# Kernel optimization log

Measured on AMD Instinct MI355X. Metric: run time of the kernel, lower is better.

Reference implementation:

```python
import jax, jax.numpy as jnp
from jax import lax
import numpy as np

B, N, C, NPOINT, K = 8, 4096, 64, 1024, 32
EPS = 1e-5
SLOPE = 0.1  # leakyrelu negative_slope


def setup_inputs() -> dict:
    key = jax.random.key(0)
    ks = jax.random.split(key, 8)
    d = {
        "xyz": jax.random.normal(ks[0], (B, N, 3), jnp.float32),
        "features": jax.random.normal(ks[1], (B, N, C), jnp.float32),
    }
    for i, n in enumerate(["w_t", "w1_0", "w2_0", "w1_1", "w2_1"]):
        d[n] = jax.random.normal(ks[2 + i], (C, C), jnp.float32) * 0.05
    for n in ["b_t", "b1_0", "b2_0", "b1_1", "b2_1"]:
        d[n] = jnp.zeros((C,), jnp.float32)
    for n in ["g_t", "g1_0", "g2_0", "g1_1", "g2_1"]:
        d[n] = jnp.ones((C,), jnp.float32)
    for n in ["beta_t", "beta1_0", "beta2_0", "beta1_1", "beta2_1"]:
        d[n] = jnp.zeros((C,), jnp.float32)
    return d


def leaky(x):
    return jnp.where(x >= 0, x, SLOPE * x)


def conv1(x, w, b):  # x: [M, Cin, K], w: [Cout, Cin] (1x1 conv)
    return jnp.einsum('mck,oc->mok', x, w) + b[None, :, None]


def bn(x, g, be):  # training-mode BatchNorm1d over (batch, spatial)
    mean = x.mean(axis=(0, 2), keepdims=True)
    var = x.var(axis=(0, 2), keepdims=True)
    return g[None, :, None] * (x - mean) / jnp.sqrt(var + EPS) + be[None, :, None]


def fps(xyz, npoint):
    """Farthest point sampling, deterministic start at index 0. -> [B, npoint] int32"""
    b, n, _ = xyz.shape
    def step(carry, _):
        dist, far = carry
        centroid = jnp.take_along_axis(xyz, far[:, None, None], axis=1)  # [B,1,3]
        d = jnp.sum((xyz - centroid) ** 2, -1)  # [B,N]
        dist = jnp.minimum(dist, d)
        return (dist, jnp.argmax(dist, -1)), far
    init = (jnp.full((b, n), 1e10, xyz.dtype), jnp.zeros((b,), jnp.int32))
    _, idxs = lax.scan(step, init, None, length=npoint)  # [npoint, B]
    return idxs.T


def sqdist(src, dst):  # [B,S,3],[B,N,3] -> [B,S,N]
    d = -2.0 * jnp.einsum('bsc,bnc->bsn', src, dst)
    d += jnp.sum(src ** 2, -1)[:, :, None]
    d += jnp.sum(dst ** 2, -1)[:, None, :]
    return d


def resblock(x, w1, b1, g1, be1, w2, b2, g2, be2):
    h = leaky(bn(conv1(x, w1, b1), g1, be1))
    h = bn(conv1(h, w2, b2), g2, be2)
    return leaky(h + x)


def reference(xyz, features, w_t, b_t, g_t, beta_t,
              w1_0, b1_0, g1_0, beta1_0, w2_0, b2_0, g2_0, beta2_0,
              w1_1, b1_1, g1_1, beta1_1, w2_1, b2_1, g2_1, beta2_1):
    fps_idx = fps(xyz, NPOINT)                                   # [B,S]
    new_xyz = jnp.take_along_axis(xyz, fps_idx[:, :, None], axis=1)  # [B,S,3]
    d = sqdist(new_xyz, xyz)                                     # [B,S,N]
    _, idx = lax.top_k(-d, K)                                    # k smallest -> [B,S,K]
    grouped = jax.vmap(lambda f, i: f[i])(features, idx)         # [B,S,K,C]
    x = grouped.transpose(0, 1, 3, 2).reshape(B * NPOINT, C, K)  # [B*S, C, K]
    x = leaky(bn(conv1(x, w_t, b_t), g_t, beta_t))
    x = resblock(x, w1_0, b1_0, g1_0, beta1_0, w2_0, b2_0, g2_0, beta2_0)
    x = resblock(x, w1_1, b1_1, g1_1, beta1_1, w2_1, b2_1, g2_1, beta2_1)
    nf = x.reshape(B, NPOINT, C, K).transpose(0, 2, 1, 3)        # [B,C,S,K]
    sub_features = nf.max(axis=-1)                               # [B,C,S]
    return (new_xyz.transpose(0, 2, 1), sub_features)
```

## Files before the change

### kernel.cpp

```cpp
#include <hip/hip_runtime.h>
#include <stdint.h>

#define NB 8
#define NN 4096
#define NC 64
#define NS 1024
#define NK 32
#define NQ (NB*NS)
#define NP (NQ*NK)
#define EPSBN 1e-5f

typedef unsigned long long u64;
typedef unsigned short u16;
typedef float v2f __attribute__((ext_vector_type(2)));
typedef short bf8_t __attribute__((ext_vector_type(8)));
typedef float f4_t __attribute__((ext_vector_type(4)));

__device__ __forceinline__ float lrelu(float x){ return x >= 0.0f ? x : 0.1f*x; }

__device__ __forceinline__ unsigned int fkey(float d){
    unsigned int fb = __float_as_uint(d);
    return (fb & 0x80000000u) ? ~fb : (fb | 0x80000000u);
}
__device__ __forceinline__ unsigned f2bf(float f){
    unsigned u = __float_as_uint(f);
    return (u + 0x7fffu + ((u >> 16) & 1u)) >> 16;
}
__device__ __forceinline__ float bflo(unsigned u){ return __uint_as_float(u << 16); }
__device__ __forceinline__ float bfhi(unsigned u){ return __uint_as_float(u & 0xffff0000u); }

__device__ __forceinline__ int wave_incl_add(int x){
    int v = x;
    {int o=__builtin_amdgcn_update_dpp(0,v,0x111,0xf,0xf,true); v+=o;}
    {int o=__builtin_amdgcn_update_dpp(0,v,0x112,0xf,0xf,true); v+=o;}
    {int o=__builtin_amdgcn_update_dpp(0,v,0x114,0xf,0xf,true); v+=o;}
    {int o=__builtin_amdgcn_update_dpp(0,v,0x118,0xf,0xf,true); v+=o;}
    {int o=__builtin_amdgcn_update_dpp(0,v,0x142,0xa,0xf,true); v+=o;}
    {int o=__builtin_amdgcn_update_dpp(0,v,0x143,0xc,0xf,true); v+=o;}
    return v;
}
__device__ __forceinline__ float row_sum16(float x){
    int v = __float_as_int(x);
    {int o=__builtin_amdgcn_update_dpp(0,v,0x111,0xf,0xf,true); v=__float_as_int(__int_as_float(v)+__int_as_float(o));}
    {int o=__builtin_amdgcn_update_dpp(0,v,0x112,0xf,0xf,true); v=__float_as_int(__int_as_float(v)+__int_as_float(o));}
    {int o=__builtin_amdgcn_update_dpp(0,v,0x114,0xf,0xf,true); v=__float_as_int(__int_as_float(v)+__int_as_float(o));}
    {int o=__builtin_amdgcn_update_dpp(0,v,0x118,0xf,0xf,true); v=__float_as_int(__int_as_float(v)+__int_as_float(o));}
    return __int_as_float(v);
}
__device__ __forceinline__ double wave_max_d(double x){
    int lo = __double2loint(x), hi = __double2hiint(x);
    #define FPS_STG(ctl) { \
        int nl=__builtin_amdgcn_update_dpp(lo,lo,ctl,0xf,0xf,false); \
        int nh=__builtin_amdgcn_update_dpp(hi,hi,ctl,0xf,0xf,false); \
        double mx=fmax(__hiloint2double(hi,lo), __hiloint2double(nh,nl)); \
        lo=__double2loint(mx); hi=__double2hiint(mx); }
    FPS_STG(0x111) FPS_STG(0x112) FPS_STG(0x114) FPS_STG(0x118) FPS_STG(0x142) FPS_STG(0x143)
    #undef FPS_STG
    int flo = __builtin_amdgcn_readlane(lo, 63);
    int fhi = __builtin_amdgcn_readlane(hi, 63);
    return __hiloint2double(fhi, flo);
}

__global__ __launch_bounds__(256,1) void fps_kernel(const float* __restrict__ xyz,
                                                    float* __restrict__ out0,
                                                    float* __restrict__ nxyz,
                                                    const float* __restrict__ features,
                                                    u16* __restrict__ fbf)
{
    if (blockIdx.x >= NB){
        const int cb = blockIdx.x - NB;
        const float4* src = (const float4*)features;
        uint2* dst = (uint2*)fbf;
        for (int i = cb*256 + threadIdx.x; i < NB*NN*NC/4; i += 512*256){
            float4 v = src[i];
            uint2 pk;
            pk.x = f2bf(v.x) | (f2bf(v.y) << 16);
            pk.y = f2bf(v.z) | (f2bf(v.w) << 16);
            dst[i] = pk;
        }
        return;
    }
    __shared__ float sX[NN], sY[NN], sZ[NN];
    __shared__ double slots[2][4];
    __shared__ int sFar[NS];
    const int b = blockIdx.x, t = threadIdx.x;
    const int lane = t & 63, wv = t >> 6;
    const float* base = xyz + (size_t)b*NN*3;
    for (int i = t; i < NN; i += 256){
        const float* pp = base + 3*i;
        sX[i] = pp[0]; sY[i] = pp[1]; sZ[i] = pp[2];
    }
    __syncthreads();
    v2f PX[8], PY[8], PZ[8], D[8];
    int LO[16];
    const int pb = t*16;
    #pragma unroll
    for (int j = 0; j < 8; ++j){
        PX[j] = (v2f){ sX[pb+2*j], sX[pb+2*j+1] };
        PY[j] = (v2f){ sY[pb+2*j], sY[pb+2*j+1] };
        PZ[j] = (v2f){ sZ[pb+2*j], sZ[pb+2*j+1] };
        D[j]  = (v2f){ 1e10f, 1e10f };
    }
    #pragma unroll
    for (int j = 0; j < 16; ++j) LO[j] = (int)(~(unsigned)(pb + j));
    int far = 0;
    float cx = sX[0], cy = sY[0], cz = sZ[0];
    for (int s = 0; s < NS; ++s){
        if (t == 255) sFar[s] = far;
        double best;
        {
            #pragma clang fp contract(off)
            v2f cx2 = (v2f){cx, cx}, cy2 = (v2f){cy, cy}, cz2 = (v2f){cz, cz};
            best = -1.0;
            #pragma unroll
            for (int j = 0; j < 8; ++j){
                v2f dx = PX[j] - cx2;
                v2f dy = PY[j] - cy2;
                v2f dz = PZ[j] - cz2;
                v2f dd = (dx*dx + dy*dy) + dz*dz;
                v2f nd = __builtin_elementwise_min(D[j], dd);
                D[j] = nd;
                best = fmax(best, __hiloint2double(__float_as_int(nd.x), LO[2*j]));
                best = fmax(best, __hiloint2double(__float_as_int(nd.y), LO[2*j+1]));
            }
        }
        double wb = wave_max_d(best);
        const int par = s & 1;
        if (lane == 0) slots[par][wv] = wb;
        __syncthreads();
        double s0 = slots[par][0], s1 = slots[par][1];
        double s2 = slots[par][2], s3 = slots[par][3];
        double mm = fmax(fmax(s0, s1), fmax(s2, s3));
        far = (int)(~(unsigned)__double2loint(mm));
        cx = sX[far]; cy = sY[far]; cz = sZ[far];
    }
    __syncthreads();
    for (int s = t; s < NS; s += 256){
        const int f = sFar[s];
        const float x = sX[f], y = sY[f], z = sZ[f];
        float* npq = nxyz + ((size_t)b*NS + s)*3;
        npq[0]=x; npq[1]=y; npq[2]=z;
        out0[(b*3+0)*NS+s]=x; out0[(b*3+1)*NS+s]=y; out0[(b*3+2)*NS+s]=z;
    }
}

__global__ __launch_bounds__(256,2) void knn_kernel(const float* __restrict__ xyz,
                                                    const float* __restrict__ nxyz,
                                                    int* __restrict__ kidx)
{
    const int t = threadIdx.x, lane = t & 63, w = t >> 6;
    const int q = blockIdx.x*4 + w;
    const int b = q >> 10;
    const float* base = xyz + (size_t)b*NN*3;
    const float* qp = nxyz + (size_t)q*3;
    const float qx = qp[0], qy = qp[1], qz = qp[2];
    const float qsq = __fadd_rn(__fadd_rn(__fmul_rn(qx,qx),__fmul_rn(qy,qy)),__fmul_rn(qz,qz));

    unsigned int key[64];
    #pragma unroll
    for (int i = 0; i < 64; ++i){
        const int idx = (i<<6) + lane;
        const float* pp = base + 3*idx;
        float x = pp[0], y = pp[1], z = pp[2];
        float dot = __fadd_rn(__fadd_rn(__fmul_rn(qx,x),__fmul_rn(qy,y)),__fmul_rn(qz,z));
        float psq = __fadd_rn(__fadd_rn(__fmul_rn(x,x),__fmul_rn(y,y)),__fmul_rn(z,z));
        float d = __fadd_rn(__fadd_rn(__fmul_rn(-2.0f,dot),qsq),psq);
        key[i] = fkey(d);
    }
    unsigned int pref = 0; int need = 32;
    for (int bit = 31; bit >= 0; --bit){
        const unsigned int bound = 1u << bit;
        int c = 0;
        #pragma unroll
        for (int i = 0; i < 64; ++i) c += ((key[i] ^ pref) < bound) ? 1 : 0;
        int tot = __builtin_amdgcn_readlane(wave_incl_add(c), 63);
        if (tot < need){ need -= tot; pref |= bound; }
    }
    const unsigned int T = pref;
    int cl = 0;
    #pragma unroll
    for (int i = 0; i < 64; ++i) cl += (key[i] < T) ? 1 : 0;
    int incl_cl = wave_incl_add(cl);
    int clx = incl_cl - cl;
    int tiebase = __builtin_amdgcn_readlane(incl_cl, 63);
    int* oq = kidx + (size_t)q*NK;
    int pos = clx;
    #pragma unroll
    for (int i = 0; i < 64; ++i){
        if (key[i] < T){ oq[pos] = (i<<6) + lane; ++pos; }
    }
    int tcount = 0;
    for (int i = 0; i < 64 && tcount < need; ++i){
        u64 m = __ballot(key[i] == T);
        int myrank = (int)__popcll(m & ((1ull << lane) - 1ull));
        if ((key[i] == T) && (tcount + myrank < need))
            oq[tiebase + tcount + myrank] = (i<<6) + lane;
        tcount += (int)__popcll(m);
    }
}

__global__ __launch_bounds__(256) void wtrans_kernel(const float* __restrict__ w0,
    const float* __restrict__ w1, const float* __restrict__ w2,
    const float* __restrict__ w3, const float* __restrict__ w4,
    u16* __restrict__ dst)
{
    const float* s;
    switch (blockIdx.x){
        case 0: s = w0; break; case 1: s = w1; break; case 2: s = w2; break;
        case 3: s = w3; break; default: s = w4; break;
    }
    u16* d = dst + (size_t)blockIdx.x*4096;
    for (int i = threadIdx.x; i < 4096; i += 256){
        const int f = i >> 9, lane = (i >> 3) & 63, j = i & 7;
        const int mt = f >> 1, h = f & 1;
        const int o = mt*16 + (lane & 15);
        const int c = h*32 + (lane >> 4)*8 + j;
        d[i] = (u16)f2bf(s[o*64 + c]);
    }
}

__global__ __launch_bounds__(1024) void finalize_kernel(const float* __restrict__ pin,
    const float* __restrict__ g, const float* __restrict__ beta, float* __restrict__ aff)
{
    __shared__ float l1[1024];
    const int t = threadIdx.x;
    const int stat = t & 127, seg = t >> 7;
    float S = 0.0f;
    #pragma unroll 8
    for (int r = seg*128; r < seg*128 + 128; ++r) S += pin[r*128 + stat];
    l1[t] = S;
    __syncthreads();
    if (t < 128){
        float s = l1[t] + l1[128+t] + l1[256+t] + l1[384+t]
                + l1[512+t] + l1[640+t] + l1[768+t] + l1[896+t];
        l1[t] = s;
    }
    __syncthreads();
    if (t < 64){
        float mean = l1[t] * (1.0f/(float)NP);
        float var  = fmaxf(l1[64+t] * (1.0f/(float)NP) - mean*mean, 0.0f);
        float sc = g[t] * rsqrtf(var + EPSBN);
        aff[t]    = sc;
        aff[64+t] = beta[t] - mean*sc;
    }
}

template<int ACT>
__global__ __launch_bounds__(256,3) void conv_mfma_kernel(const u16* __restrict__ in,
    u16* __restrict__ out, const u16* __restrict__ wfrag, const float* __restrict__ bias,
    const float* __restrict__ aff, float* __restrict__ pout)
{
    __shared__ float sStat[4*128];
    const int t = threadIdx.x, lane = t & 63, wv = t >> 6;
    const int n = lane & 15, q = lane >> 4;
    const int bb = blockIdx.x;

    float scr[16], shr[16];
    if (ACT){
        #pragma unroll
        for (int h = 0; h < 2; ++h){
            float4 a0 = *(const float4*)(aff + h*32 + q*8);
            float4 a1 = *(const float4*)(aff + h*32 + q*8 + 4);
            float4 b0 = *(const float4*)(aff + 64 + h*32 + q*8);
            float4 b1 = *(const float4*)(aff + 64 + h*32 + q*8 + 4);
            scr[h*8+0]=a0.x; scr[h*8+1]=a0.y; scr[h*8+2]=a0.z; scr[h*8+3]=a0.w;
            scr[h*8+4]=a1.x; scr[h*8+5]=a1.y; scr[h*8+6]=a1.z; scr[h*8+7]=a1.w;
            shr[h*8+0]=b0.x; shr[h*8+1]=b0.y; shr[h*8+2]=b0.z; shr[h*8+3]=b0.w;
            shr[h*8+4]=b1.x; shr[h*8+5]=b1.y; shr[h*8+6]=b1.z; shr[h*8+7]=b1.w;
        }
    }
    bf8_t wf[8];
    #pragma unroll
    for (int f = 0; f < 8; ++f)
        wf[f] = *(const bf8_t*)(wfrag + (f*64 + lane)*8);
    f4_t bv[4];
    #pragma unroll
    for (int mt = 0; mt < 4; ++mt)
        bv[mt] = *(const f4_t*)(bias + mt*16 + q*4);

    float st1[16], st2[16];
    #pragma unroll
    for (int e = 0; e < 16; ++e){ st1[e] = 0.0f; st2[e] = 0.0f; }

    #pragma unroll
    for (int i = 0; i < 4; ++i){
        const int p0 = bb*256 + wv*64 + i*16;
        const u16* row = in + (size_t)(p0 + n)*64;
        bf8_t bf0, bf1;
        if (ACT){
            union { unsigned u[4]; bf8_t v; } B0, B1;
            uint4 r0 = *(const uint4*)(row + q*8);
            uint4 r1 = *(const uint4*)(row + 32 + q*8);
            const unsigned ra[4] = {r0.x, r0.y, r0.z, r0.w};
            const unsigned rb[4] = {r1.x, r1.y, r1.z, r1.w};
            #pragma unroll
            for (int d = 0; d < 4; ++d){
                float x0 = bflo(ra[d]), x1 = bfhi(ra[d]);
                float y0 = fmaf(scr[2*d],   x0, shr[2*d]);   y0 = lrelu(y0);
                float y1 = fmaf(scr[2*d+1], x1, shr[2*d+1]); y1 = lrelu(y1);
                B0.u[d] = f2bf(y0) | (f2bf(y1) << 16);
                float z0 = bflo(rb[d]), z1 = bfhi(rb[d]);
                float w0 = fmaf(scr[8+2*d],   z0, shr[8+2*d]);   w0 = lrelu(w0);
                float w1 = fmaf(scr[8+2*d+1], z1, shr[8+2*d+1]); w1 = lrelu(w1);
                B1.u[d] = f2bf(w0) | (f2bf(w1) << 16);
            }
            bf0 = B0.v; bf1 = B1.v;
        } else {
            bf0 = *(const bf8_t*)(row + q*8);
            bf1 = *(const bf8_t*)(row + 32 + q*8);
        }
        f4_t acc[4];
        #pragma unroll
        for (int mt = 0; mt < 4; ++mt){
            acc[mt] = (f4_t){0.f,0.f,0.f,0.f};
            acc[mt] = __builtin_amdgcn_mfma_f32_16x16x32_bf16(wf[mt*2+0], bf0, acc[mt], 0,0,0);
            acc[mt] = __builtin_amdgcn_mfma_f32_16x16x32_bf16(wf[mt*2+1], bf1, acc[mt], 0,0,0);
        }
        u16* orow = out + (size_t)(p0 + n)*64;
        #pragma unroll
        for (int mt = 0; mt < 4; ++mt){
            float v0 = acc[mt].x + bv[mt].x;
            float v1 = acc[mt].y + bv[mt].y;
            float v2 = acc[mt].z + bv[mt].z;
            float v3 = acc[mt].w + bv[mt].w;
            st1[mt*4+0] += v0; st2[mt*4+0] += v0*v0;
            st1[mt*4+1] += v1; st2[mt*4+1] += v1*v1;
            st1[mt*4+2] += v2; st2[mt*4+2] += v2*v2;
            st1[mt*4+3] += v3; st2[mt*4+3] += v3*v3;
            uint2 pk;
            pk.x = f2bf(v0) | (f2bf(v1) << 16);
            pk.y = f2bf(v2) | (f2bf(v3) << 16);
            *(uint2*)(orow + mt*16 + q*4) = pk;
        }
    }
    #pragma unroll
    for (int e = 0; e < 16; ++e){
        float r1 = row_sum16(st1[e]);
        float r2 = row_sum16(st2[e]);
        if (n == 15){
            const int ch = (e >> 2)*16 + q*4 + (e & 3);
            sStat[wv*128 + ch]      = r1;
            sStat[wv*128 + 64 + ch] = r2;
        }
    }
    __syncthreads();
    if (t < 128){
        float s = sStat[t] + sStat[128+t] + sStat[256+t] + sStat[384+t];
        pout[(size_t)bb*128 + t] = s;
    }
}

__global__ __launch_bounds__(256,3) void gconv_mfma_kernel(const u16* __restrict__ fbf,
    const int* __restrict__ kidx, u16* __restrict__ out,
    const u16* __restrict__ wfrag, const float* __restrict__ bias,
    float* __restrict__ pout)
{
    __shared__ float sStat[4*128];
    const int t = threadIdx.x, lane = t & 63, wv = t >> 6;
    const int n = lane & 15, q = lane >> 4;
    const int bb = blockIdx.x;

    bf8_t wf[8];
    #pragma unroll
    for (int f = 0; f < 8; ++f)
        wf[f] = *(const bf8_t*)(wfrag + (f*64 + lane)*8);
    f4_t bv[4];
    #pragma unroll
    for (int mt = 0; mt < 4; ++mt)
        bv[mt] = *(const f4_t*)(bias + mt*16 + q*4);

    float st1[16], st2[16];
    #pragma unroll
    for (int e = 0; e < 16; ++e){ st1[e] = 0.0f; st2[e] = 0.0f; }

    #pragma unroll
    for (int i = 0; i < 4; ++i){
        const int p0 = bb*256 + wv*64 + i*16;
        const int p = p0 + n;
        const int b = p >> 15;
        const int idx = kidx[p];
        const u16* frow = fbf + ((size_t)b*NN + idx)*NC;
        bf8_t bf0 = *(const bf8_t*)(frow + q*8);
        bf8_t bf1 = *(const bf8_t*)(frow + 32 + q*8);
        f4_t acc[4];
        #pragma unroll
        for (int mt = 0; mt < 4; ++mt){
            acc[mt] = (f4_t){0.f,0.f,0.f,0.f};
            acc[mt] = __builtin_amdgcn_mfma_f32_16x16x32_bf16(wf[mt*2+0], bf0, acc[mt], 0,0,0);
            acc[mt] = __builtin_amdgcn_mfma_f32_16x16x32_bf16(wf[mt*2+1], bf1, acc[mt], 0,0,0);
        }
        u16* orow = out + (size_t)p*64;
        #pragma unroll
        for (int mt = 0; mt < 4; ++mt){
            float v0 = acc[mt].x + bv[mt].x;
            float v1 = acc[mt].y + bv[mt].y;
            float v2 = acc[mt].z + bv[mt].z;
            float v3 = acc[mt].w + bv[mt].w;
            st1[mt*4+0] += v0; st2[mt*4+0] += v0*v0;
            st1[mt*4+1] += v1; st2[mt*4+1] += v1*v1;
            st1[mt*4+2] += v2; st2[mt*4+2] += v2*v2;
            st1[mt*4+3] += v3; st2[mt*4+3] += v3*v3;
            uint2 pk;
            pk.x = f2bf(v0) | (f2bf(v1) << 16);
            pk.y = f2bf(v2) | (f2bf(v3) << 16);
            *(uint2*)(orow + mt*16 + q*4) = pk;
        }
    }
    #pragma unroll
    for (int e = 0; e < 16; ++e){
        float r1 = row_sum16(st1[e]);
        float r2 = row_sum16(st2[e]);
        if (n == 15){
            const int ch = (e >> 2)*16 + q*4 + (e & 3);
            sStat[wv*128 + ch]      = r1;
            sStat[wv*128 + 64 + ch] = r2;
        }
    }
    __syncthreads();
    if (t < 128){
        float s = sStat[t] + sStat[128+t] + sStat[256+t] + sStat[384+t];
        pout[(size_t)bb*128 + t] = s;
    }
}

__global__ __launch_bounds__(256,2) void resid_kernel(const u16* __restrict__ v,
    const u16* __restrict__ yt, u16* __restrict__ x2,
    const float* __restrict__ affV, const float* __restrict__ affY)
{
    const int t = threadIdx.x;
    const int dc = t & 31, rg = t >> 5;
    const int c0 = dc*2, c1 = c0 + 1;
    const float va0 = affV[c0], vb0 = affV[64+c0];
    const float va1 = affV[c1], vb1 = affV[64+c1];
    const float ya0 = affY[c0], yb0 = affY[64+c0];
    const float ya1 = affY[c1], yb1 = affY[64+c1];
    const unsigned* vp = (const unsigned*)v;
    const unsigned* yp = (const unsigned*)yt;
    unsigned* xp = (unsigned*)x2;
    const size_t base = (size_t)blockIdx.x*512;
    #pragma unroll 4
    for (int r = rg; r < 512; r += 8){
        const size_t e = (base + r)*32 + dc;
        unsigned uv = vp[e], uy = yp[e];
        float r0 = lrelu(fmaf(va0, bflo(uv), vb0) + lrelu(fmaf(ya0, bflo(uy), yb0)));
        float r1 = lrelu(fmaf(va1, bfhi(uv), vb1) + lrelu(fmaf(ya1, bfhi(uy), yb1)));
        xp[e] = f2bf(r0) | (f2bf(r1) << 16);
    }
}

__global__ __launch_bounds__(256,2) void final_kernel(const u16* __restrict__ v2,
    const u16* __restrict__ x2, const float* __restrict__ aff,
    float* __restrict__ out1)
{
    const int t = threadIdx.x;
    const int dc = t & 31, sg = t >> 5;
    const int c0 = dc*2, c1 = c0 + 1;
    const float a0 = aff[c0], s0 = aff[64+c0];
    const float a1 = aff[c1], s1 = aff[64+c1];
    const int s = blockIdx.x*8 + sg;
    const unsigned* vp = (const unsigned*)v2;
    const unsigned* xp = (const unsigned*)x2;
    float m0 = -3.0e38f, m1 = -3.0e38f;
    #pragma unroll 8
    for (int kk = 0; kk < 32; ++kk){
        const size_t e = ((size_t)s*32 + kk)*32 + dc;
        unsigned uv = vp[e], ux = xp[e];
        m0 = fmaxf(m0, lrelu(fmaf(a0, bflo(uv), s0) + bflo(ux)));
        m1 = fmaxf(m1, lrelu(fmaf(a1, bfhi(uv), s1) + bfhi(ux)));
    }
    const int b = s >> 10, sl = s & 1023;
    out1[((size_t)b*NC + c0)*NS + sl] = m0;
    out1[((size_t)b*NC + c1)*NS + sl] = m1;
}

extern "C" void kernel_launch(void* const* d_in, const int* in_sizes, int n_in,
                              void* d_out, int out_size, void* d_ws, size_t ws_size,
                              hipStream_t stream)
{
    const float* xyz      = (const float*)d_in[0];
    const float* features = (const float*)d_in[1];
    const float* w_t    = (const float*)d_in[2];
    const float* w1_0   = (const float*)d_in[3];
    const float* w2_0   = (const float*)d_in[4];
    const float* w1_1   = (const float*)d_in[5];
    const float* w2_1   = (const float*)d_in[6];
    const float* b_t    = (const float*)d_in[7];
    const float* b1_0   = (const float*)d_in[8];
    const float* b2_0   = (const float*)d_in[9];
    const float* b1_1   = (const float*)d_in[10];
    const float* b2_1   = (const float*)d_in[11];
    const float* g_t    = (const float*)d_in[12];
    const float* g1_0   = (const float*)d_in[13];
    const float* g2_0   = (const float*)d_in[14];
    const float* g1_1   = (const float*)d_in[15];
    const float* g2_1   = (const float*)d_in[16];
    const float* beta_t  = (const float*)d_in[17];
    const float* beta1_0 = (const float*)d_in[18];
    const float* beta2_0 = (const float*)d_in[19];
    const float* beta1_1 = (const float*)d_in[20];
    const float* beta2_1 = (const float*)d_in[21];

    float* out = (float*)d_out;

    float* nxyz = (float*)d_ws;
    int*   kidx = (int*)(nxyz + 24576);
    float* pT   = (float*)(kidx + NP);
    float* p10  = pT  + 131072;
    float* p20  = p10 + 131072;
    float* p11  = p20 + 131072;
    float* p21  = p11 + 131072;
    float* affT  = p21 + 131072;
    float* aff10 = affT + 128;
    float* aff20 = aff10 + 128;
    float* aff11 = aff20 + 128;
    float* aff21 = aff11 + 128;
    u16*  bwt  = (u16*)(aff21 + 128);
    u16*  buf0 = bwt + 5*4096;
    u16*  buf1 = buf0 + (size_t)NP*NC;
    u16*  buf2 = buf1 + (size_t)NP*NC;
    u16*  fbf  = buf2;

    wtrans_kernel<<<5, 256, 0, stream>>>(w_t, w1_0, w2_0, w1_1, w2_1, bwt);
    fps_kernel<<<NB + 512, 256, 0, stream>>>(xyz, out, nxyz, features, fbf);
    knn_kernel<<<NQ/4, 256, 0, stream>>>(xyz, nxyz, kidx);

    gconv_mfma_kernel<<<1024, 256, 0, stream>>>(fbf, kidx, buf1,
                                                bwt + 0*4096, b_t, pT);
    finalize_kernel<<<1, 1024, 0, stream>>>(pT, g_t, beta_t, affT);
    conv_mfma_kernel<1><<<1024, 256, 0, stream>>>(buf1, buf0, bwt + 1*4096, b1_0,
                                                  affT, p10);
    finalize_kernel<<<1, 1024, 0, stream>>>(p10, g1_0, beta1_0, aff10);
    conv_mfma_kernel<1><<<1024, 256, 0, stream>>>(buf0, buf2, bwt + 2*4096, b2_0,
                                                  aff10, p20);
    finalize_kernel<<<1, 1024, 0, stream>>>(p20, g2_0, beta2_0, aff20);
    resid_kernel<<<512, 256, 0, stream>>>(buf2, buf1, buf0, aff20, affT);
    conv_mfma_kernel<0><<<1024, 256, 0, stream>>>(buf0, buf1, bwt + 3*4096, b1_1,
                                                  nullptr, p11);
    finalize_kernel<<<1, 1024, 0, stream>>>(p11, g1_1, beta1_1, aff11);
    conv_mfma_kernel<1><<<1024, 256, 0, stream>>>(buf1, buf2, bwt + 4*4096, b2_1,
                                                  aff11, p21);
    finalize_kernel<<<1, 1024, 0, stream>>>(p21, g2_1, beta2_1, aff21);
    final_kernel<<<1024, 256, 0, stream>>>(buf2, buf0, aff21,
                                           out + (size_t)NB*3*NS);
}
```

Baseline: 905.8 us.

## Fuse BN finalize into conv tails, fold residual into conv, merge weight prep

```diff
diff --git a/kernel.cpp b/kernel.cpp
--- a/kernel.cpp
+++ b/kernel.cpp
@@ -61,12 +61,71 @@
     return __hiloint2double(fhi, flo);
 }
 
+__device__ __forceinline__ void tail_finalize(const float* __restrict__ pin,
+    const float* __restrict__ g, const float* __restrict__ beta,
+    float* __restrict__ affout, int* __restrict__ ticket, int t)
+{
+    __shared__ int isTail;
+    __shared__ float l1[1024];
+    __threadfence();
+    __syncthreads();
+    if (t == 0) isTail = ((atomicAdd(ticket, 1) & 1023) == 1023) ? 1 : 0;
+    __syncthreads();
+    if (!isTail) return;
+    __threadfence();
+    const float4* p4 = (const float4*)pin;
+    const int col4 = t & 31, seg = t >> 5;
+    float4 S = {0.f, 0.f, 0.f, 0.f};
+    #pragma unroll 8
+    for (int r = seg*128; r < seg*128 + 128; ++r){
+        float4 v = p4[(size_t)r*32 + col4];
+        S.x += v.x; S.y += v.y; S.z += v.z; S.w += v.w;
+    }
+    l1[seg*128 + col4*4 + 0] = S.x;
+    l1[seg*128 + col4*4 + 1] = S.y;
+    l1[seg*128 + col4*4 + 2] = S.z;
+    l1[seg*128 + col4*4 + 3] = S.w;
+    __syncthreads();
+    if (t < 128){
+        float s = l1[t] + l1[128+t] + l1[256+t] + l1[384+t]
+                + l1[512+t] + l1[640+t] + l1[768+t] + l1[896+t];
+        l1[t] = s;
+    }
+    __syncthreads();
+    if (t < 64){
+        float mean = l1[t] * (1.0f/(float)NP);
+        float var  = fmaxf(l1[64+t] * (1.0f/(float)NP) - mean*mean, 0.0f);
+        float sc = g[t] * rsqrtf(var + EPSBN);
+        affout[t]    = sc;
+        affout[64+t] = beta[t] - mean*sc;
+    }
+}
+
 __global__ __launch_bounds__(256,1) void fps_kernel(const float* __restrict__ xyz,
-                                                    float* __restrict__ out0,
-                                                    float* __restrict__ nxyz,
-                                                    const float* __restrict__ features,
-                                                    u16* __restrict__ fbf)
-{
+    float* __restrict__ out0, float* __restrict__ nxyz,
+    const float* __restrict__ features, u16* __restrict__ fbf,
+    const float* __restrict__ w0, const float* __restrict__ w1,
+    const float* __restrict__ w2, const float* __restrict__ w3,
+    const float* __restrict__ w4, u16* __restrict__ bwt, int* __restrict__ tickets)
+{
+    if (blockIdx.x >= NB + 512){
+        const int wb = blockIdx.x - (NB + 512);
+        if (wb == 0 && threadIdx.x < 8) tickets[threadIdx.x] = 0;
+        const float* s;
+        switch (wb){
+            case 0: s = w0; break; case 1: s = w1; break; case 2: s = w2; break;
+            case 3: s = w3; break; default: s = w4; break;
+        }
+        u16* d = bwt + (size_t)wb*4096;
+        for (int i = threadIdx.x; i < 4096; i += 256){
+            const int f = i >> 9, lane = (i >> 3) & 63, j = i & 7;
+            const int mt = f >> 1, h = f & 1;
+            const int o = mt*16 + (lane & 15);
+            const int c = h*32 + (lane >> 4)*8 + j;
+            d[i] = (u16)f2bf(s[o*64 + c]);
+        }
+        return;
+    }
     if (blockIdx.x >= NB){
         const int cb = blockIdx.x - NB;
         const float4* src = (const float4*)features;
@@ -199,56 +258,15 @@
     }
 }
 
-__global__ __launch_bounds__(256) void wtrans_kernel(const float* __restrict__ w0,
-    const float* __restrict__ w1, const float* __restrict__ w2,
-    const float* __restrict__ w3, const float* __restrict__ w4,
-    u16* __restrict__ dst)
-{
-    const float* s;
-    switch (blockIdx.x){
-        case 0: s = w0; break; case 1: s = w1; break; case 2: s = w2; break;
-        case 3: s = w3; break; default: s = w4; break;
-    }
-    u16* d = dst + (size_t)blockIdx.x*4096;
-    for (int i = threadIdx.x; i < 4096; i += 256){
-        const int f = i >> 9, lane = (i >> 3) & 63, j = i & 7;
-        const int mt = f >> 1, h = f & 1;
-        const int o = mt*16 + (lane & 15);
-        const int c = h*32 + (lane >> 4)*8 + j;
-        d[i] = (u16)f2bf(s[o*64 + c]);
-    }
-}
-
-__global__ __launch_bounds__(1024) void finalize_kernel(const float* __restrict__ pin,
-    const float* __restrict__ g, const float* __restrict__ beta, float* __restrict__ aff)
-{
-    __shared__ float l1[1024];
-    const int t = threadIdx.x;
-    const int stat = t & 127, seg = t >> 7;
-    float S = 0.0f;
-    #pragma unroll 8
-    for (int r = seg*128; r < seg*128 + 128; ++r) S += pin[r*128 + stat];
-    l1[t] = S;
-    __syncthreads();
-    if (t < 128){
-        float s = l1[t] + l1[128+t] + l1[256+t] + l1[384+t]
-                + l1[512+t] + l1[640+t] + l1[768+t] + l1[896+t];
-        l1[t] = s;
-    }
-    __syncthreads();
-    if (t < 64){
-        float mean = l1[t] * (1.0f/(float)NP);
-        float var  = fmaxf(l1[64+t] * (1.0f/(float)NP) - mean*mean, 0.0f);
-        float sc = g[t] * rsqrtf(var + EPSBN);
-        aff[t]    = sc;
-        aff[64+t] = beta[t] - mean*sc;
-    }
-}
-
 template<int ACT>
-__global__ __launch_bounds__(256,3) void conv_mfma_kernel(const u16* __restrict__ in,
-    u16* __restrict__ out, const u16* __restrict__ wfrag, const float* __restrict__ bias,
-    const float* __restrict__ aff, float* __restrict__ pout)
+__global__ __launch_bounds__(256, (ACT==2)?2:3) void conv_mfma_kernel(
+    const u16* __restrict__ in, const u16* __restrict__ in2,
+    u16* __restrict__ out, u16* __restrict__ x2out,
+    const u16* __restrict__ wfrag, const float* __restrict__ bias,
+    const float* __restrict__ aff, const float* __restrict__ aff2,
+    float* __restrict__ pout, const float* __restrict__ g,
+    const float* __restrict__ beta, float* __restrict__ affout,
+    int* __restrict__ ticket)
 {
     __shared__ float sStat[4*128];
     const int t = threadIdx.x, lane = t & 63, wv = t >> 6;
@@ -256,7 +274,8 @@
     const int bb = blockIdx.x;
 
     float scr[16], shr[16];
-    if (ACT){
+    float scr2[16], shr2[16];
+    {
         #pragma unroll
         for (int h = 0; h < 2; ++h){
             float4 a0 = *(const float4*)(aff + h*32 + q*8);
@@ -268,6 +287,19 @@
             shr[h*8+0]=b0.x; shr[h*8+1]=b0.y; shr[h*8+2]=b0.z; shr[h*8+3]=b0.w;
             shr[h*8+4]=b1.x; shr[h*8+5]=b1.y; shr[h*8+6]=b1.z; shr[h*8+7]=b1.w;
         }
+        if (ACT == 2){
+            #pragma unroll
+            for (int h = 0; h < 2; ++h){
+                float4 a0 = *(const float4*)(aff2 + h*32 + q*8);
+                float4 a1 = *(const float4*)(aff2 + h*32 + q*8 + 4);
+                float4 b0 = *(const float4*)(aff2 + 64 + h*32 + q*8);
+                float4 b1 = *(const float4*)(aff2 + 64 + h*32 + q*8 + 4);
+                scr2[h*8+0]=a0.x; scr2[h*8+1]=a0.y; scr2[h*8+2]=a0.z; scr2[h*8+3]=a0.w;
+                scr2[h*8+4]=a1.x; scr2[h*8+5]=a1.y; scr2[h*8+6]=a1.z; scr2[h*8+7]=a1.w;
+                shr2[h*8+0]=b0.x; shr2[h*8+1]=b0.y; shr2[h*8+2]=b0.z; shr2[h*8+3]=b0.w;
+                shr2[h*8+4]=b1.x; shr2[h*8+5]=b1.y; shr2[h*8+6]=b1.z; shr2[h*8+7]=b1.w;
+            }
+        }
     }
     bf8_t wf[8];
     #pragma unroll
@@ -287,8 +319,8 @@
         const int p0 = bb*256 + wv*64 + i*16;
         const u16* row = in + (size_t)(p0 + n)*64;
         bf8_t bf0, bf1;
-        if (ACT){
-            union { unsigned u[4]; bf8_t v; } B0, B1;
+        union { unsigned u[4]; bf8_t v; } B0, B1;
+        if (ACT == 1){
             uint4 r0 = *(const uint4*)(row + q*8);
             uint4 r1 = *(const uint4*)(row + 32 + q*8);
             const unsigned ra[4] = {r0.x, r0.y, r0.z, r0.w};
@@ -306,8 +338,32 @@
             }
             bf0 = B0.v; bf1 = B1.v;
         } else {
-            bf0 = *(const bf8_t*)(row + q*8);
-            bf1 = *(const bf8_t*)(row + 32 + q*8);
+            const u16* yrow = in2 + (size_t)(p0 + n)*64;
+            uint4 r0 = *(const uint4*)(row + q*8);
+            uint4 r1 = *(const uint4*)(row + 32 + q*8);
+            uint4 s0 = *(const uint4*)(yrow + q*8);
+            uint4 s1 = *(const uint4*)(yrow + 32 + q*8);
+            const unsigned ra[4] = {r0.x, r0.y, r0.z, r0.w};
+            const unsigned rb[4] = {r1.x, r1.y, r1.z, r1.w};
+            const unsigned ya[4] = {s0.x, s0.y, s0.z, s0.w};
+            const unsigned yb[4] = {s1.x, s1.y, s1.z, s1.w};
+            #pragma unroll
+            for (int d = 0; d < 4; ++d){
+                float t0 = lrelu(fmaf(scr2[2*d],   bflo(ya[d]), shr2[2*d]));
+                float t1 = lrelu(fmaf(scr2[2*d+1], bfhi(ya[d]), shr2[2*d+1]));
+                float x0 = lrelu(fmaf(scr[2*d],    bflo(ra[d]), shr[2*d])   + t0);
+                float x1 = lrelu(fmaf(scr[2*d+1],  bfhi(ra[d]), shr[2*d+1]) + t1);
+                B0.u[d] = f2bf(x0) | (f2bf(x1) << 16);
+                float u0 = lrelu(fmaf(scr2[8+2*d],   bflo(yb[d]), shr2[8+2*d]));
+                float u1 = lrelu(fmaf(scr2[8+2*d+1], bfhi(yb[d]), shr2[8+2*d+1]));
+                float v0 = lrelu(fmaf(scr[8+2*d],    bflo(rb[d]), shr[8+2*d])   + u0);
+                float v1 = lrelu(fmaf(scr[8+2*d+1],  bfhi(rb[d]), shr[8+2*d+1]) + u1);
+                B1.u[d] = f2bf(v0) | (f2bf(v1) << 16);
+            }
+            u16* xrow = x2out + (size_t)(p0 + n)*64;
+            *(uint4*)(xrow + q*8)      = r0 = (uint4){B0.u[0],B0.u[1],B0.u[2],B0.u[3]};
+            *(uint4*)(xrow + 32 + q*8) = r1 = (uint4){B1.u[0],B1.u[1],B1.u[2],B1.u[3]};
+            bf0 = B0.v; bf1 = B1.v;
         }
         f4_t acc[4];
         #pragma unroll
@@ -348,12 +404,15 @@
         float s = sStat[t] + sStat[128+t] + sStat[256+t] + sStat[384+t];
         pout[(size_t)bb*128 + t] = s;
     }
+    tail_finalize(pout, g, beta, affout, ticket, t);
 }
 
 __global__ __launch_bounds__(256,3) void gconv_mfma_kernel(const u16* __restrict__ fbf,
     const int* __restrict__ kidx, u16* __restrict__ out,
     const u16* __restrict__ wfrag, const float* __restrict__ bias,
-    float* __restrict__ pout)
+    float* __restrict__ pout, const float* __restrict__ g,
+    const float* __restrict__ beta, float* __restrict__ affout,
+    int* __restrict__ ticket)
 {
     __shared__ float sStat[4*128];
     const int t = threadIdx.x, lane = t & 63, wv = t >> 6;
@@ -421,31 +480,7 @@
         float s = sStat[t] + sStat[128+t] + sStat[256+t] + sStat[384+t];
         pout[(size_t)bb*128 + t] = s;
     }
-}
-
-__global__ __launch_bounds__(256,2) void resid_kernel(const u16* __restrict__ v,
-    const u16* __restrict__ yt, u16* __restrict__ x2,
-    const float* __restrict__ affV, const float* __restrict__ affY)
-{
-    const int t = threadIdx.x;
-    const int dc = t & 31, rg = t >> 5;
-    const int c0 = dc*2, c1 = c0 + 1;
-    const float va0 = affV[c0], vb0 = affV[64+c0];
-    const float va1 = affV[c1], vb1 = affV[64+c1];
-    const float ya0 = affY[c0], yb0 = affY[64+c0];
-    const float ya1 = affY[c1], yb1 = affY[64+c1];
-    const unsigned* vp = (const unsigned*)v;
-    const unsigned* yp = (const unsigned*)yt;
-    unsigned* xp = (unsigned*)x2;
-    const size_t base = (size_t)blockIdx.x*512;
-    #pragma unroll 4
-    for (int r = rg; r < 512; r += 8){
-        const size_t e = (base + r)*32 + dc;
-        unsigned uv = vp[e], uy = yp[e];
-        float r0 = lrelu(fmaf(va0, bflo(uv), vb0) + lrelu(fmaf(ya0, bflo(uy), yb0)));
-        float r1 = lrelu(fmaf(va1, bfhi(uv), vb1) + lrelu(fmaf(ya1, bfhi(uy), yb1)));
-        xp[e] = f2bf(r0) | (f2bf(r1) << 16);
-    }
+    tail_finalize(pout, g, beta, affout, ticket, t);
 }
 
 __global__ __launch_bounds__(256,2) void final_kernel(const u16* __restrict__ v2,
@@ -514,32 +549,37 @@
     float* aff20 = aff10 + 128;
     float* aff11 = aff20 + 128;
     float* aff21 = aff11 + 128;
-    u16*  bwt  = (u16*)(aff21 + 128);
+    int*  tickets = (int*)(aff21 + 128);
+    u16*  bwt  = (u16*)(tickets + 8);
     u16*  buf0 = bwt + 5*4096;
     u16*  buf1 = buf0 + (size_t)NP*NC;
     u16*  buf2 = buf1 + (size_t)NP*NC;
     u16*  fbf  = buf2;
 
-    wtrans_kernel<<<5, 256, 0, stream>>>(w_t, w1_0, w2_0, w1_1, w2_1, bwt);
-    fps_kernel<<<NB + 512, 256, 0, stream>>>(xyz, out, nxyz, features, fbf);
+    fps_kernel<<<NB + 512 + 5, 256, 0, stream>>>(xyz, out, nxyz, features, fbf,
+                                                 w_t, w1_0, w2_0, w1_1, w2_1,
+                                                 bwt, tickets);
     knn_kernel<<<NQ/4, 256, 0, stream>>>(xyz, nxyz, kidx);
 
     gconv_mfma_kernel<<<1024, 256, 0, stream>>>(fbf, kidx, buf1,
-                                                bwt + 0*4096, b_t, pT);
-    finalize_kernel<<<1, 1024, 0, stream>>>(pT, g_t, beta_t, affT);
-    conv_mfma_kernel<1><<<1024, 256, 0, stream>>>(buf1, buf0, bwt + 1*4096, b1_0,
-                                                  affT, p10);
-    finalize_kernel<<<1, 1024, 0, stream>>>(p10, g1_0, beta1_0, aff10);
-    conv_mfma_kernel<1><<<1024, 256, 0, stream>>>(buf0, buf2, bwt + 2*4096, b2_0,
-                                                  aff10, p20);
-    finalize_kernel<<<1, 1024, 0, stream>>>(p20, g2_0, beta2_0, aff20);
-    resid_kernel<<<512, 256, 0, stream>>>(buf2, buf1, buf0, aff20, affT);
-    conv_mfma_kernel<0><<<1024, 256, 0, stream>>>(buf0, buf1, bwt + 3*4096, b1_1,
-                                                  nullptr, p11);
-    finalize_kernel<<<1, 1024, 0, stream>>>(p11, g1_1, beta1_1, aff11);
-    conv_mfma_kernel<1><<<1024, 256, 0, stream>>>(buf1, buf2, bwt + 4*4096, b2_1,
-                                                  aff11, p21);
-    finalize_kernel<<<1, 1024, 0, stream>>>(p21, g2_1, beta2_1, aff21);
+                                                bwt + 0*4096, b_t,
+                                                pT, g_t, beta_t, affT, tickets + 0);
+    conv_mfma_kernel<1><<<1024, 256, 0, stream>>>(buf1, nullptr, buf0, nullptr,
+                                                  bwt + 1*4096, b1_0,
+                                                  affT, nullptr,
+                                                  p10, g1_0, beta1_0, aff10, tickets + 1);
+    conv_mfma_kernel<1><<<1024, 256, 0, stream>>>(buf0, nullptr, buf2, nullptr,
+                                                  bwt + 2*4096, b2_0,
+                                                  aff10, nullptr,
+                                                  p20, g2_0, beta2_0, aff20, tickets + 2);
+    conv_mfma_kernel<2><<<1024, 256, 0, stream>>>(buf2, buf1, buf1, buf0,
+                                                  bwt + 3*4096, b1_1,
+                                                  aff20, affT,
+                                                  p11, g1_1, beta1_1, aff11, tickets + 3);
+    conv_mfma_kernel<1><<<1024, 256, 0, stream>>>(buf1, nullptr, buf2, nullptr,
+                                                  bwt + 4*4096, b2_1,
+                                                  aff11, nullptr,
+                                                  p21, g2_1, beta2_1, aff21, tickets + 4);
     final_kernel<<<1024, 256, 0, stream>>>(buf2, buf0, aff21,
                                            out + (size_t)NB*3*NS);
 }
```

New measurement: 1.563 ms. +72.5%, slower.
